# Kernel optimization log

Measured on AMD Instinct MI355X. Metric: run time of the kernel, lower is better.

Reference implementation:

```python
import jax, jax.numpy as jnp
import numpy as np

B, S, L, D = 16, 16, 128, 768   # batch, num_sentences, max_sentence_length, hidden_size
A, T = 8, 5                      # num_args, max_arg_length
VOCAB = 500                      # small id range so arg tokens actually match


def setup_inputs() -> dict:
    key = jax.random.key(0)
    k0, k1, k2, k3, k4, k5 = jax.random.split(key, 6)
    hidden_states = jax.random.normal(k0, (B, S, L, D), dtype=jnp.float32)
    sentence_ids = jax.random.randint(k1, (B, S, L), 0, VOCAB, dtype=jnp.int64)
    # realistic attention masks: ones on a prefix of each sentence
    lens = jax.random.randint(k2, (B, S, 1), L // 2, L + 1)
    sentence_attention_masks = (jnp.arange(L)[None, None, :] < lens).astype(jnp.int32)
    predicate_ids = jax.random.randint(k3, (B, S, A, T), 0, VOCAB, dtype=jnp.int64)
    arg0_ids = jax.random.randint(k4, (B, S, A, T), 0, VOCAB, dtype=jnp.int64)
    arg1_ids = jax.random.randint(k5, (B, S, A, T), 0, VOCAB, dtype=jnp.int64)
    return {
        "hidden_states": hidden_states,
        "sentence_ids": sentence_ids,
        "sentence_attention_masks": sentence_attention_masks,
        "predicate_ids": predicate_ids,
        "arg0_ids": arg0_ids,
        "arg1_ids": arg1_ids,
    }


def _arg_embedding(arg_ids, sentence_ids, hidden):
    # match[b,s,a,t,l] = (sentence token l equals arg token t)
    match = sentence_ids[:, :, None, None, :] == arg_ids[..., None]          # [B,S,A,T,L] bool
    counts = match.sum(-1)                                                   # [B,S,A,T]
    matchf = match.astype(hidden.dtype)
    # per-arg-token mean over matching sentence positions
    avg = jnp.einsum('bsatl,bsld->bsatd', matchf, hidden)
    avg = avg / jnp.maximum(counts, 1).astype(hidden.dtype)[..., None]       # [B,S,A,T,D]
    # torch loop overwrites per token -> keep LAST nonzero token with a match
    valid = (arg_ids != 0) & (counts > 0)                                    # [B,S,A,T]
    Tn = arg_ids.shape[-1]
    last = Tn - 1 - jnp.argmax(valid[..., ::-1].astype(jnp.int32), axis=-1)  # [B,S,A]
    gathered = jnp.take_along_axis(avg, last[..., None, None], axis=3)[..., 0, :]
    return jnp.where(valid.any(-1)[..., None], gathered, jnp.zeros((), hidden.dtype))


def reference(hidden_states, sentence_ids, sentence_attention_masks,
              predicate_ids, arg0_ids, arg1_ids):
    # mean pooling over valid tokens
    m = sentence_attention_masks.astype(hidden_states.dtype)                 # [B,S,L]
    summed = jnp.einsum('bsl,bsld->bsd', m, hidden_states)
    counts = jnp.maximum(m.sum(-1, keepdims=True), 1.0)
    sentence_embeddings_avg = summed / counts                                # [B,S,D]
    predicate_embeddings = _arg_embedding(predicate_ids, sentence_ids, hidden_states)
    arg0_embeddings = _arg_embedding(arg0_ids, sentence_ids, hidden_states)
    arg1_embeddings = _arg_embedding(arg1_ids, sentence_ids, hidden_states)
    return (sentence_embeddings_avg, predicate_embeddings, arg0_embeddings, arg1_embeddings)
```

## Files before the change

### kernel.cpp

```cpp
#include <hip/hip_runtime.h>


namespace {
constexpr int Bc = 16, Sc = 16, Lc = 128, Dc = 768, Ac = 8, Tc = 5;
constexpr int NF4    = Dc / 4;
constexpr int CHUNK  = 32;
constexpr int NCHUNK = NF4 / CHUNK;
constexpr int BLOCK  = 256;
constexpr int RP     = BLOCK / CHUNK;
constexpr int NSLOT  = 3 * Ac;
constexpr int OUT1   = Bc * Sc * NF4;
constexpr int OUTG   = Bc * Sc * Ac * NF4;
}

__global__ __launch_bounds__(BLOCK) void srl_fused(
    const float4* __restrict__ hid,
    const int*    __restrict__ sids,
    const int*    __restrict__ amask,
    const int*    __restrict__ pids,
    const int*    __restrict__ a0ids,
    const int*    __restrict__ a1ids,
    float4*       __restrict__ out)
{
  const int c   = blockIdx.x;
  const int bs  = blockIdx.y;
  const int tid = threadIdx.x;
  const int q   = tid & (CHUNK - 1);
  const int r   = tid >> 5;

  __shared__ int    sid[Lc];
  __shared__ short  slist[NSLOT][Lc];
  __shared__ int    scnt[NSLOT];
  __shared__ float4 red[BLOCK];

  int mval = 0;
  if (tid < Lc) {
    sid[tid] = sids[bs * Lc + tid];
    mval     = amask[bs * Lc + tid];
  }
  const int len = __syncthreads_count(mval != 0);

  const float4* __restrict__ hrow = hid + (size_t)bs * Lc * NF4 + c * CHUNK;

  if (tid < NSLOT) {
    const int g = tid / Ac, a = tid % Ac;
    const int* ids = (g == 0 ? pids : (g == 1 ? a0ids : a1ids)) + (bs * Ac + a) * Tc;
    int tok[Tc], cnt[Tc];
#pragma unroll
    for (int t = 0; t < Tc; ++t) { tok[t] = ids[t]; cnt[t] = 0; }
    for (int l = 0; l < Lc; ++l) {
      const int v = sid[l];
#pragma unroll
      for (int t = 0; t < Tc; ++t) cnt[t] += (v == tok[t]) ? 1 : 0;
    }
    int sel = 0, n = 0;
#pragma unroll
    for (int t = Tc - 1; t >= 0; --t) {
      if (n == 0 && tok[t] != 0 && cnt[t] > 0) { sel = tok[t]; n = cnt[t]; }
    }
    scnt[tid] = n;
    if (n > 0) {
      int k = 0;
      for (int l = 0; l < Lc; ++l)
        if (sid[l] == sel) slist[tid][k++] = (short)l;
    }
  }

  float ax = 0.f, ay = 0.f, az = 0.f, aw = 0.f;
#pragma unroll 4
  for (int l = r; l < len; l += RP) {
    const float4 v = hrow[l * NF4 + q];
    ax += v.x; ay += v.y; az += v.z; aw += v.w;
  }
  red[tid] = make_float4(ax, ay, az, aw);
  __syncthreads();

  if (tid < CHUNK) {
    float4 s = red[q];
#pragma unroll
    for (int p = 1; p < RP; ++p) {
      const float4 t = red[p * CHUNK + q];
      s.x += t.x; s.y += t.y; s.z += t.z; s.w += t.w;
    }
    const float inv = 1.0f / (float)(len > 0 ? len : 1);
    s.x *= inv; s.y *= inv; s.z *= inv; s.w *= inv;
    out[bs * NF4 + c * CHUNK + q] = s;
  }

  for (int j = r; j < NSLOT; j += RP) {
    const int n = scnt[j];
    float ox = 0.f, oy = 0.f, oz = 0.f, ow = 0.f;
    if (n > 0) {
      for (int i = 0; i < n; ++i) {
        const int l = (int)slist[j][i];
        const float4 v = hrow[l * NF4 + q];
        ox += v.x; oy += v.y; oz += v.z; ow += v.w;
      }
      const float inv = 1.0f / (float)n;
      ox *= inv; oy *= inv; oz *= inv; ow *= inv;
    }
    const int g = j / Ac, a = j % Ac;
    out[OUT1 + g * OUTG + (bs * Ac + a) * NF4 + c * CHUNK + q] =
        make_float4(ox, oy, oz, ow);
  }
}

extern "C" void kernel_launch(void* const* d_in, const int* in_sizes, int n_in,
                              void* d_out, int out_size, void* d_ws, size_t ws_size,
                              hipStream_t stream) {
  const float4* hid   = (const float4*)d_in[0];
  const int*    sids  = (const int*)d_in[1];
  const int*    amask = (const int*)d_in[2];
  const int*    pids  = (const int*)d_in[3];
  const int*    a0ids = (const int*)d_in[4];
  const int*    a1ids = (const int*)d_in[5];
  float4*       out   = (float4*)d_out;

  srl_fused<<<dim3(NCHUNK, Bc * Sc), dim3(BLOCK), 0, stream>>>(
      hid, sids, amask, pids, a0ids, a1ids, out);
}
```

Baseline: 159.0 us.

## Parallelize arg-token matching with wave ballots and halve per-block column chunk

Replaces the serial per-slot scan, where 24 threads each loop over 128 tokens, with a parallel match count. Each of 128 threads compares its sentence token against all 120 arg tokens using wave ballots and atomic adds. Match lists are then built in parallel with atomics after an extra barrier. The column chunk is halved to 16 float4s, which doubles the grid and the number of rows handled per block. This cuts the serial setup latency but adds barriers and makes each memory row access narrower.

```diff
diff --git a/kernel.cpp b/kernel.cpp
--- a/kernel.cpp
+++ b/kernel.cpp
@@ -4,11 +4,12 @@
 namespace {
 constexpr int Bc = 16, Sc = 16, Lc = 128, Dc = 768, Ac = 8, Tc = 5;
 constexpr int NF4    = Dc / 4;
-constexpr int CHUNK  = 32;
+constexpr int CHUNK  = 16;
 constexpr int NCHUNK = NF4 / CHUNK;
 constexpr int BLOCK  = 256;
 constexpr int RP     = BLOCK / CHUNK;
 constexpr int NSLOT  = 3 * Ac;
+constexpr int NTOK   = NSLOT * Tc;
 constexpr int OUT1   = Bc * Sc * NF4;
 constexpr int OUTG   = Bc * Sc * Ac * NF4;
 }
@@ -26,45 +27,32 @@
   const int bs  = blockIdx.y;
   const int tid = threadIdx.x;
   const int q   = tid & (CHUNK - 1);
-  const int r   = tid >> 5;
+  const int r   = tid >> 4;
 
-  __shared__ int    sid[Lc];
-  __shared__ short  slist[NSLOT][Lc];
-  __shared__ int    scnt[NSLOT];
-  __shared__ float4 red[BLOCK];
+  __shared__ int     sid[Lc];
+  __shared__ int     tok_s[NTOK];
+  __shared__ int     cnt_s[NTOK];
+  __shared__ int     sel_s[NSLOT];
+  __shared__ int     scnt_s[NSLOT];
+  __shared__ int     lpos_s[NSLOT];
+  __shared__ unsigned char slist[NSLOT][Lc];
+  __shared__ float4  red[BLOCK];
 
   int mval = 0;
   if (tid < Lc) {
     sid[tid] = sids[bs * Lc + tid];
     mval     = amask[bs * Lc + tid];
+  } else if (tid < Lc + NTOK) {
+    const int k   = tid - Lc;
+    const int g   = k / (Ac * Tc);
+    const int rem = k - g * (Ac * Tc);
+    const int* ids = (g == 0 ? pids : (g == 1 ? a0ids : a1ids));
+    tok_s[k] = ids[bs * Ac * Tc + rem];
+    cnt_s[k] = 0;
   }
   const int len = __syncthreads_count(mval != 0);
 
   const float4* __restrict__ hrow = hid + (size_t)bs * Lc * NF4 + c * CHUNK;
-
-  if (tid < NSLOT) {
-    const int g = tid / Ac, a = tid % Ac;
-    const int* ids = (g == 0 ? pids : (g == 1 ? a0ids : a1ids)) + (bs * Ac + a) * Tc;
-    int tok[Tc], cnt[Tc];
-#pragma unroll
-    for (int t = 0; t < Tc; ++t) { tok[t] = ids[t]; cnt[t] = 0; }
-    for (int l = 0; l < Lc; ++l) {
-      const int v = sid[l];
-#pragma unroll
-      for (int t = 0; t < Tc; ++t) cnt[t] += (v == tok[t]) ? 1 : 0;
-    }
-    int sel = 0, n = 0;
-#pragma unroll
-    for (int t = Tc - 1; t >= 0; --t) {
-      if (n == 0 && tok[t] != 0 && cnt[t] > 0) { sel = tok[t]; n = cnt[t]; }
-    }
-    scnt[tid] = n;
-    if (n > 0) {
-      int k = 0;
-      for (int l = 0; l < Lc; ++l)
-        if (sid[l] == sel) slist[tid][k++] = (short)l;
-    }
-  }
 
   float ax = 0.f, ay = 0.f, az = 0.f, aw = 0.f;
 #pragma unroll 4
@@ -73,22 +61,57 @@
     ax += v.x; ay += v.y; az += v.z; aw += v.w;
   }
   red[tid] = make_float4(ax, ay, az, aw);
+
+  if (tid < Lc) {
+    const int  v     = sid[tid];
+    const bool lane0 = ((tid & 63) == 0);
+    for (int k = 0; k < NTOK; ++k) {
+      const unsigned long long m = __ballot(v == tok_s[k]);
+      if (lane0 && m) atomicAdd(&cnt_s[k], __popcll(m));
+    }
+  }
   __syncthreads();
 
   if (tid < CHUNK) {
-    float4 s = red[q];
+    float4 s = red[tid];
 #pragma unroll
     for (int p = 1; p < RP; ++p) {
-      const float4 t = red[p * CHUNK + q];
+      const float4 t = red[p * CHUNK + tid];
       s.x += t.x; s.y += t.y; s.z += t.z; s.w += t.w;
     }
     const float inv = 1.0f / (float)(len > 0 ? len : 1);
     s.x *= inv; s.y *= inv; s.z *= inv; s.w *= inv;
-    out[bs * NF4 + c * CHUNK + q] = s;
+    out[bs * NF4 + c * CHUNK + tid] = s;
   }
+  else if (tid >= 64 && tid < 64 + NSLOT) {
+    const int j = tid - 64;
+    int selv = -1, n = 0;
+#pragma unroll
+    for (int t = Tc - 1; t >= 0; --t) {
+      const int tokv = tok_s[j * Tc + t];
+      const int cv   = cnt_s[j * Tc + t];
+      if (n == 0 && tokv != 0 && cv > 0) { selv = tokv; n = cv; }
+    }
+    sel_s[j]  = selv;
+    scnt_s[j] = n;
+    lpos_s[j] = 0;
+  }
+  __syncthreads();
+
+  if (tid < Lc) {
+    const int v = sid[tid];
+#pragma unroll
+    for (int j = 0; j < NSLOT; ++j) {
+      if (v == sel_s[j]) {
+        const int p = atomicAdd(&lpos_s[j], 1);
+        slist[j][p] = (unsigned char)tid;
+      }
+    }
+  }
+  __syncthreads();
 
   for (int j = r; j < NSLOT; j += RP) {
-    const int n = scnt[j];
+    const int n = scnt_s[j];
     float ox = 0.f, oy = 0.f, oz = 0.f, ow = 0.f;
     if (n > 0) {
       for (int i = 0; i < n; ++i) {
@@ -99,7 +122,7 @@
       const float inv = 1.0f / (float)n;
       ox *= inv; oy *= inv; oz *= inv; ow *= inv;
     }
-    const int g = j / Ac, a = j % Ac;
+    const int g = j / Ac, a = j - g * Ac;
     out[OUT1 + g * OUTG + (bs * Ac + a) * NF4 + c * CHUNK + q] =
         make_float4(ox, oy, oz, ow);
   }
```

Result: slower. 170.0 us (+6.9%).
